# Kernel optimization log

Hardware: AMD Instinct MI355X
Metric: run time of the kernel (lower is better)

Reference implementation:

```python
import jax, jax.numpy as jnp
import numpy as np

E = 20000      # num edges
S = 64         # mul of 0e (scalar) channels
V = 32         # mul of 1o (vector) channels
FC_IN = 128    # radial basis length
HID = 64       # fc hidden width
INV_SQRT3 = 0.5773502691896258  # CG(1o x 1o -> 0e) = delta_ij / sqrt(3)


def setup_inputs() -> dict:
    key = jax.random.key(0)
    ks = jax.random.split(key, 16)
    n = jax.random.normal
    return {
        # edge features, layout [64 scalars | 32 vectors * 3 comps]
        "fea_in1": n(ks[0], (E, S + 3 * V), jnp.float32),
        "fea_in2": n(ks[1], (E, S + 3 * V), jnp.float32),
        "fea_weight": n(ks[2], (E, FC_IN), jnp.float32),
        # FullyConnectedTensorProduct internal weights (e3nn init: normal(0,1))
        "w_ss_s": n(ks[3], (S, S, S), jnp.float32),   # 0e x 0e -> 64x0e scalars
        "w_vv_s": n(ks[4], (V, V, S), jnp.float32),   # 1o x 1o -> 64x0e scalars
        "w_ss_g": n(ks[5], (S, S, V), jnp.float32),   # 0e x 0e -> 32x0e gates
        "w_vv_g": n(ks[6], (V, V, V), jnp.float32),   # 1o x 1o -> 32x0e gates
        "w_sv_v": n(ks[7], (S, V, V), jnp.float32),   # 0e x 1o -> 32x1o
        "w_vs_v": n(ks[8], (V, S, V), jnp.float32),   # 1o x 0e -> 32x1o
        # fc MLP: Linear(128,64) SiLU Linear(64,64) SiLU Linear(64,96)
        "fc_w1": n(ks[9], (FC_IN, HID), jnp.float32) / np.sqrt(FC_IN).astype(np.float32),
        "fc_b1": jnp.zeros((HID,), jnp.float32),
        "fc_w2": n(ks[10], (HID, HID), jnp.float32) / np.sqrt(HID).astype(np.float32),
        "fc_b2": jnp.zeros((HID,), jnp.float32),
        "fc_w3": n(ks[11], (HID, S + V), jnp.float32) / np.sqrt(HID).astype(np.float32),
        "fc_b3": jnp.zeros((S + V,), jnp.float32),
        "batch_edge": jnp.zeros((E,), jnp.int32),  # unused (norm='')
    }


def _equiconv(fea_in1, fea_in2, fea_weight,
              w_ss_s, w_vv_s, w_ss_g, w_vv_g, w_sv_v, w_vs_v,
              fc_w1, fc_b1, fc_w2, fc_b2, fc_w3, fc_b3):
    x1s, x1v = fea_in1[:, :S], fea_in1[:, S:].reshape(-1, V, 3)
    x2s, x2v = fea_in2[:, :S], fea_in2[:, S:].reshape(-1, V, 3)

    # path normalization: 1/sqrt(fan_in), fan_in = sum(mul1*mul2) over paths to output
    a_sc = 1.0 / np.sqrt(S * S + V * V).astype(np.float32)
    a_vec = 1.0 / np.sqrt(2 * S * V).astype(np.float32)

    # FullyConnectedTensorProduct (uvw connectivity)
    sc = a_sc * (jnp.einsum('eu,ev,uvw->ew', x1s, x2s, w_ss_s)
                 + INV_SQRT3 * jnp.einsum('eui,evi,uvw->ew', x1v, x2v, w_vv_s))
    g = a_sc * (jnp.einsum('eu,ev,uvw->ew', x1s, x2s, w_ss_g)
                + INV_SQRT3 * jnp.einsum('eui,evi,uvw->ew', x1v, x2v, w_vv_g))
    vec = a_vec * (jnp.einsum('eu,evi,uvw->ewi', x1s, x2v, w_sv_v)
                   + jnp.einsum('eui,ev,uvw->ewi', x1v, x2s, w_vs_v))

    # Gate: silu on scalars, sigmoid gates multiply the l>0 part
    sc = jax.nn.silu(sc)
    vec = vec * jax.nn.sigmoid(g)[:, :, None]

    # fc MLP producing per-channel elementwise conv weights
    h = jax.nn.silu(fea_weight @ fc_w1 + fc_b1)
    h = jax.nn.silu(h @ fc_w2 + fc_b2)
    w = h @ fc_w3 + fc_b3  # [E, S+V]

    # e3ElementWise: one scalar weight per channel (shared over m components)
    sc = sc * w[:, :S]
    vec = vec * w[:, S:, None]
    return jnp.concatenate([sc, vec.reshape(-1, 3 * V)], axis=-1)


def reference(fea_in1, fea_in2, fea_weight,
              w_ss_s, w_vv_s, w_ss_g, w_vv_g, w_sv_v, w_vs_v,
              fc_w1, fc_b1, fc_w2, fc_b2, fc_w3, fc_b3, batch_edge):
    del batch_edge  # only used by optional e3LayerNorm (norm='')
    return _equiconv(fea_in1, fea_in2, fea_weight,
                     w_ss_s, w_vv_s, w_ss_g, w_vv_g, w_sv_v, w_vs_v,
                     fc_w1, fc_b1, fc_w2, fc_b2, fc_w3, fc_b3)
```

## Files before the change

### kernel.cpp

```cpp
#include <hip/hip_runtime.h>


#define E_TOT 20000

typedef __attribute__((ext_vector_type(8))) short short8;
typedef __attribute__((ext_vector_type(4))) float f32x4;
typedef __attribute__((ext_vector_type(2))) __bf16 bf16x2;

#define FRAG_USH 512
#define CH_USH   3072
#define N_CH     52
#define STRIDE_W 159744
#define FC1_OFF  638976
#define FC2_OFF  647168
#define FC3_OFF  651264
#define WS_USH   657408

#define X1S_OFF  30720
#define X1V_OFF  34944
#define POOL_B   41216

__device__ __forceinline__ unsigned short f2b(float f){
  return __builtin_bit_cast(unsigned short, (__bf16)f);
}
__device__ __forceinline__ unsigned f2b2(float lo, float hi){
  bf16x2 t; t[0] = (__bf16)lo; t[1] = (__bf16)hi;
  return __builtin_bit_cast(unsigned, t);
}
__device__ __forceinline__ float b2f(unsigned short h){
  return __uint_as_float(((unsigned)h) << 16);
}
__device__ __forceinline__ float ulo(unsigned u){ return __uint_as_float(u << 16); }
__device__ __forceinline__ float uhi(unsigned u){ return __uint_as_float(u & 0xFFFF0000u); }
__device__ __forceinline__ f32x4 mfma16(short8 a, short8 b, f32x4 c){
  return __builtin_amdgcn_mfma_f32_16x16x32_bf16(a, b, c, 0, 0, 0);
}
union U8 { short8 v; unsigned u[4]; };
__device__ __forceinline__ float silu_f(float x){ return x/(1.f+__expf(-x)); }
__device__ __forceinline__ float sigm_f(float x){ return 1.f/(1.f+__expf(-x)); }

#define PACK8P(a, s, xp) { \
  a.u[0]=f2b2((s)*ulo((xp)[0]),(s)*uhi((xp)[0])); \
  a.u[1]=f2b2((s)*ulo((xp)[1]),(s)*uhi((xp)[1])); \
  a.u[2]=f2b2((s)*ulo((xp)[2]),(s)*uhi((xp)[2])); \
  a.u[3]=f2b2((s)*ulo((xp)[3]),(s)*uhi((xp)[3])); }

__device__ __forceinline__ int fpos(int kl, int n16){
  return (kl>>3)*128 + n16*8 + (kl&7);
}

__global__ void prep_weights(const float* __restrict__ ss_s, const float* __restrict__ ss_g,
                             const float* __restrict__ vv_s, const float* __restrict__ vv_g,
                             const float* __restrict__ sv,   const float* __restrict__ vs,
                             const float* __restrict__ w1,   const float* __restrict__ w2,
                             const float* __restrict__ w3,   unsigned short* __restrict__ wsb)
{
  int g = blockIdx.x * 256 + threadIdx.x;
  if (g >= WS_USH/8) return;
  const int dest = g << 3;
  const float A_SC  = 0.013975424859373686f;
  const float A_VV  = (float)(0.013975424859373686 * 0.5773502691896258);
  const float A_VEC = 0.015625f;

  const float* src = nullptr;
  int stride = 0;
  float scale = 1.f;

  if (dest < FC1_OFF) {
    int wave = dest / STRIDE_W;
    int off  = dest - wave*STRIDE_W;
    int c    = off / CH_USH;
    int rem  = off - c*CH_USH;
    int t    = rem >> 9;
    int p    = rem & 511;
    int kl   = (p >> 7) << 3;
    int n16  = (p >> 3) & 15;
    if (c < 32) {
      int u = (wave<<4) + (c>>1);
      int v = ((c&1)<<5) + kl;
      if (t < 4) { src = ss_s + (u<<12)+(v<<6)+((t<<4)+n16);     stride = 64; }
      else       { src = ss_g + (u<<11)+(v<<5)+(((t-4)<<4)+n16); stride = 32; }
      scale = A_SC;
    } else if (c < 40) {
      int u = (wave<<3) + (c-32);
      int v = kl;
      if (t < 4) { src = vv_s + (u<<11)+(v<<6)+((t<<4)+n16);     stride = 64; }
      else       { src = vv_g + (u<<10)+(v<<5)+(((t-4)<<4)+n16); stride = 32; }
      scale = A_VV;
    } else if (c < 46) {
      int ul = (c-40)*3 + (t>>1);
      if (ul < 16) {
        int u = (wave<<4) + ul;
        src = sv + (u<<10)+(kl<<5)+(((t&1)<<4)+n16);
        stride = 32; scale = A_VEC;
      }
    } else {
      int cc = c - 46;
      int vh = cc/3, ch3 = cc - vh*3;
      int fseq = ch3*6 + t;
      if (fseq < 16) {
        int u = (wave<<3) + (fseq>>1);
        int v = (vh<<5) + kl;
        src = vs + (u<<11)+(v<<5)+(((fseq&1)<<4)+n16);
        stride = 32; scale = A_VEC;
      }
    }
  } else if (dest < FC2_OFF) {
    int off = dest - FC1_OFF;
    int fi = off >> 9, p = off & 511;
    int kl = (p>>7)<<3, n16 = (p>>3)&15;
    int k = ((fi>>2)<<5) + kl, n = ((fi&3)<<4) + n16;
    src = w1 + (k<<6) + n; stride = 64;
  } else if (dest < FC3_OFF) {
    int off = dest - FC2_OFF;
    int fi = off >> 9, p = off & 511;
    int kl = (p>>7)<<3, n16 = (p>>3)&15;
    int k = ((fi>>2)<<5) + kl, n = ((fi&3)<<4) + n16;
    src = w2 + (k<<6) + n; stride = 64;
  } else {
    int off = dest - FC3_OFF;
    int fi = off >> 9, p = off & 511;
    int kl = (p>>7)<<3, n16 = (p>>3)&15;
    int koff = fi/6, nhi = fi - koff*6;
    int k = (koff<<5) + kl, n = (nhi<<4) + n16;
    src = w3 + k*96 + n; stride = 96;
  }

  U8 a;
  if (src) {
    float v0 = scale * src[0*stride], v1 = scale * src[1*stride];
    float v2 = scale * src[2*stride], v3 = scale * src[3*stride];
    float v4 = scale * src[4*stride], v5 = scale * src[5*stride];
    float v6 = scale * src[6*stride], v7 = scale * src[7*stride];
    a.u[0] = f2b2(v0, v1); a.u[1] = f2b2(v2, v3);
    a.u[2] = f2b2(v4, v5); a.u[3] = f2b2(v6, v7);
  } else {
    a.u[0] = 0; a.u[1] = 0; a.u[2] = 0; a.u[3] = 0;
  }
  *(short8*)(wsb + dest) = a.v;
}

__global__ __launch_bounds__(256, 2)
void equiconv_main(const float* __restrict__ fea1,
                   const float* __restrict__ fea2,
                   const float* __restrict__ few,
                   const float* __restrict__ fb1,
                   const float* __restrict__ fb2,
                   const float* __restrict__ fb3,
                   const unsigned short* __restrict__ wsb,
                   float* __restrict__ out)
{
  __shared__ __align__(16) unsigned char pool[POOL_B];
  float*          redf = (float*)pool;
  unsigned short* x1s_ = (unsigned short*)(pool + X1S_OFF);
  unsigned short* x1v_ = (unsigned short*)(pool + X1V_OFF);
  unsigned short* hb_  = (unsigned short*)(pool + X1S_OFF);

  #define X1S(r, cc) x1s_[(r)*66 + (cc)]
  #define X1V(r, cc) x1v_[(r)*98 + (cc)]
  #define HB(w, r, cc) hb_[(((w)<<4) + (r))*72 + (cc)]

  const int tid  = threadIdx.x;
  const int lane = tid & 63, wv = tid >> 6;
  const int ln   = lane & 15, quad = lane >> 4, q8 = quad << 3;
  const int ebase = blockIdx.x << 5;

  const int off16 = blockIdx.x & 15;
  const int off8  = blockIdx.x & 7;
  const int off6  = blockIdx.x % 6;

  for (int it = tid; it < 1280; it += 256){
    int row = it / 40, seg = it - row*40;
    float4 v1 = *(const float4*)(fea1 + (size_t)(ebase + row)*160 + seg*4);
    const float* p1 = (const float*)&v1;
    int c0 = seg*4;
    #pragma unroll
    for (int jj = 0; jj < 4; jj++){
      int col = c0 + jj;
      if (col < 64) X1S(row, col) = f2b(p1[jj]);
      else          X1V(row, col-64) = f2b(p1[jj]);
    }
  }
  __syncthreads();

  unsigned xep[2][4], xop[2][4], y0p[2][4], y1p[2][4], y2p[2][4];
  #pragma unroll
  for (int s = 0; s < 2; s++){
    const float* p = fea2 + (size_t)(ebase + s*16 + ln)*160;
    float4 a0 = *(const float4*)(p + q8);
    float4 a1 = *(const float4*)(p + q8 + 4);
    float4 b0 = *(const float4*)(p + 32 + q8);
    float4 b1 = *(const float4*)(p + 36 + q8);
    xep[s][0]=f2b2(a0.x,a0.y); xep[s][1]=f2b2(a0.z,a0.w);
    xep[s][2]=f2b2(a1.x,a1.y); xep[s][3]=f2b2(a1.z,a1.w);
    xop[s][0]=f2b2(b0.x,b0.y); xop[s][1]=f2b2(b0.z,b0.w);
    xop[s][2]=f2b2(b1.x,b1.y); xop[s][3]=f2b2(b1.z,b1.w);
    const float* py = p + 64 + q8*3;
    float yb[24];
    #pragma unroll
    for (int t = 0; t < 12; t++){
      float2 f2v = *(const float2*)(py + 2*t);
      yb[2*t] = f2v.x; yb[2*t+1] = f2v.y;
    }
    #pragma unroll
    for (int q = 0; q < 4; q++){
      y0p[s][q] = f2b2(yb[6*q+0], yb[6*q+3]);
      y1p[s][q] = f2b2(yb[6*q+1], yb[6*q+4]);
      y2p[s][q] = f2b2(yb[6*q+2], yb[6*q+5]);
    }
  }

  const unsigned short* gstream = wsb + (size_t)wv*STRIDE_W + lane*8;
  auto LD = [&](int c, short8* buf){
    const unsigned short* g = gstream + c*CH_USH;
    #pragma unroll
    for (int t = 0; t < 6; t++) buf[t] = *(const short8*)(g + t*FRAG_USH);
  };

  const int r0 = ln, r1 = 16 + ln;
  const f32x4 z4 = {0.f,0.f,0.f,0.f};
  f32x4 accS[2][6] = {{z4,z4,z4,z4,z4,z4},{z4,z4,z4,z4,z4,z4}};
  f32x4 accV[2][3][2] = {{{z4,z4},{z4,z4},{z4,z4}},{{z4,z4},{z4,z4},{z4,z4}}};

  short8 bA[6], bB[6];
  LD(2*off16, bA);

  #pragma unroll 1
  for (int i = 0; i < 16; i++){
    int p  = (i + off16) & 15;
    int pn = (i + 1 + off16) & 15;
    int u = (wv<<4) + p;
    float s0 = b2f(X1S(r0, u));
    float s1 = b2f(X1S(r1, u));
    {
      LD(2*p+1, bB);
      U8 a0, a1;
      PACK8P(a0, s0, xep[0]); PACK8P(a1, s1, xep[1]);
      #pragma unroll
      for (int t = 0; t < 6; t++){
        accS[0][t] = mfma16(a0.v, bA[t], accS[0][t]);
        accS[1][t] = mfma16(a1.v, bA[t], accS[1][t]);
      }
    }
    {
      int nextc = (i < 15) ? 2*pn : (32 + off8);
      LD(nextc, bA);
      U8 a0, a1;
      PACK8P(a0, s0, xop[0]); PACK8P(a1, s1, xop[1]);
      #pragma unroll
      for (int t = 0; t < 6; t++){
        accS[0][t] = mfma16(a0.v, bB[t], accS[0][t]);
        accS[1][t] = mfma16(a1.v, bB[t], accS[1][t]);
      }
    }
  }
  #define VVA(uV, s, aa) { \
    int rr = (s) ? r1 : r0; \
    float c0 = b2f(X1V(rr, (uV)*3+0)); \
    float c1 = b2f(X1V(rr, (uV)*3+1)); \
    float c2 = b2f(X1V(rr, (uV)*3+2)); \
    _Pragma("unroll") \
    for (int q = 0; q < 4; q++){ \
      float lo = c0*ulo(y0p[s][q]) + c1*ulo(y1p[s][q]) + c2*ulo(y2p[s][q]); \
      float hi = c0*uhi(y0p[s][q]) + c1*uhi(y1p[s][q]) + c2*uhi(y2p[s][q]); \
      aa.u[q] = f2b2(lo, hi); \
    } }
  #pragma unroll 1
  for (int j = 0; j < 8; j += 2){
    int k0 = (j + off8) & 7;
    int k1 = (j + 1 + off8) & 7;
    int k2 = (j + 2 + off8) & 7;
    {
      LD(32+k1, bB);
      int u = (wv<<3) + k0;
      U8 a0, a1; VVA(u, 0, a0); VVA(u, 1, a1);
      #pragma unroll
      for (int t = 0; t < 6; t++){
        accS[0][t] = mfma16(a0.v, bA[t], accS[0][t]);
        accS[1][t] = mfma16(a1.v, bA[t], accS[1][t]);
      }
    }
    {
      int nextc = (j < 6) ? (32 + k2) : (40 + off6);
      LD(nextc, bA);
      int u = (wv<<3) + k1;
      U8 a0, a1; VVA(u, 0, a0); VVA(u, 1, a1);
      #pragma unroll
      for (int t = 0; t < 6; t++){
        accS[0][t] = mfma16(a0.v, bB[t], accS[0][t]);
        accS[1][t] = mfma16(a1.v, bB[t], accS[1][t]);
      }
    }
  }
  #define SVBODY(chv, buf) { \
    _Pragma("unroll") \
    for (int uu = 0; uu < 3; uu++){ \
      int ui = (chv)*3 + uu; \
      if (ui < 16){ \
        int u = (wv<<4) + ui; \
        float s0 = b2f(X1S(r0, u)); \
        float s1 = b2f(X1S(r1, u)); \
        U8 a[2][3]; \
        PACK8P(a[0][0], s0, y0p[0]); PACK8P(a[0][1], s0, y1p[0]); PACK8P(a[0][2], s0, y2p[0]); \
        PACK8P(a[1][0], s1, y0p[1]); PACK8P(a[1][1], s1, y1p[1]); PACK8P(a[1][2], s1, y2p[1]); \
        _Pragma("unroll") \
        for (int t = 0; t < 2; t++){ \
          short8 b8 = buf[uu*2 + t]; \
          _Pragma("unroll") \
          for (int s = 0; s < 2; s++) \
            _Pragma("unroll") \
            for (int i2 = 0; i2 < 3; i2++) \
              accV[s][i2][t] = mfma16(a[s][i2].v, b8, accV[s][i2][t]); \
        } \
      } \
    } }
  #pragma unroll 1
  for (int j = 0; j < 6; j += 2){
    int c0i = j + off6;     if (c0i >= 6) c0i -= 6;
    int c1i = j + 1 + off6; if (c1i >= 6) c1i -= 6;
    int c2i = j + 2 + off6; if (c2i >= 6) c2i -= 6;
    { LD(40 + c1i, bB); SVBODY(c0i, bA); }
    {
      int nextc = (j < 4) ? (40 + c2i) : (46 + off6);
      LD(nextc, bA);
      SVBODY(c1i, bB);
    }
  }
  #define VSBODY(pcv, buf) { \
    const int p_ = (pcv)/3, ch_ = (pcv) - p_*3; \
    _Pragma("unroll") \
    for (int uu = 0; uu < 3; uu++){ \
      int ui = ch_*3 + uu; \
      if (ui < 8){ \
        int u = (wv<<3) + ui; \
        U8 a[2][3]; \
        _Pragma("unroll") \
        for (int s = 0; s < 2; s++){ \
          int rr = s ? r1 : r0; \
          float c0 = b2f(X1V(rr, u*3+0)); \
          float c1 = b2f(X1V(rr, u*3+1)); \
          float c2 = b2f(X1V(rr, u*3+2)); \
          const unsigned* xx = p_ ? xop[s] : xep[s]; \
          PACK8P(a[s][0], c0, xx); PACK8P(a[s][1], c1, xx); PACK8P(a[s][2], c2, xx); \
        } \
        _Pragma("unroll") \
        for (int t = 0; t < 2; t++){ \
          short8 b8 = buf[uu*2 + t]; \
          _Pragma("unroll") \
          for (int s = 0; s < 2; s++) \
            _Pragma("unroll") \
            for (int i2 = 0; i2 < 3; i2++) \
              accV[s][i2][t] = mfma16(a[s][i2].v, b8, accV[s][i2][t]); \
        } \
      } \
    } }
  #pragma unroll 1
  for (int j = 0; j < 6; j += 2){
    int c0i = j + off6;     if (c0i >= 6) c0i -= 6;
    int c1i = j + 1 + off6; if (c1i >= 6) c1i -= 6;
    int c2i = j + 2 + off6; if (c2i >= 6) c2i -= 6;
    { LD(46 + c1i, bB); VSBODY(c0i, bA); }
    {
      if (j < 4) LD(46 + c2i, bA);
      VSBODY(c1i, bB);
    }
  }

  f32x4 T0[12], T1[12];
  #pragma unroll
  for (int t = 0; t < 6; t++){ T0[t] = accS[0][t]; T1[t] = accS[1][t]; }
  #pragma unroll
  for (int t = 0; t < 2; t++)
    #pragma unroll
    for (int i = 0; i < 3; i++){
      T0[6+3*t+i] = accV[0][i][t]; T1[6+3*t+i] = accV[1][i][t];
    }

  #define PUT12(base, T) { _Pragma("unroll") for (int j=0;j<12;j++) \
    *(f32x4*)(redf + ((base)+j)*320 + ln*20 + (quad<<2)) = T[j]; }
  #define ADD12(base, T) { _Pragma("unroll") for (int j=0;j<12;j++) \
    T[j] += *(const f32x4*)(redf + ((base)+j)*320 + ln*20 + (quad<<2)); }

  __syncthreads();
  if (wv==1) PUT12(0, T0);  if (wv==2) PUT12(12, T1);
  __syncthreads();
  if (wv==0) ADD12(0, T0);  if (wv==3) ADD12(12, T1);
  __syncthreads();
  if (wv==2) PUT12(0, T0);  if (wv==1) PUT12(12, T1);
  __syncthreads();
  if (wv==0) ADD12(0, T0);  if (wv==3) ADD12(12, T1);
  __syncthreads();
  if (wv==3) PUT12(0, T0);  if (wv==0) PUT12(12, T1);
  __syncthreads();
  if (wv==0) ADD12(0, T0);  if (wv==3) ADD12(12, T1);

  if (wv == 1 || wv == 2) return;
  const int s = (wv == 0) ? 0 : 1;
  f32x4* P = (wv == 0) ? T0 : T1;

  f32x4 accF[4] = {z4,z4,z4,z4};
  {
    const float* fwp = few + (size_t)(ebase + s*16 + ln)*128;
    const short8* B = (const short8*)(wsb + FC1_OFF);
    #pragma unroll
    for (int c = 0; c < 4; c++){
      float4 fa  = *(const float4*)(fwp + c*32 + q8);
      float4 fbv = *(const float4*)(fwp + c*32 + q8 + 4);
      U8 a;
      a.u[0]=f2b2(fa.x,fa.y);   a.u[1]=f2b2(fa.z,fa.w);
      a.u[2]=f2b2(fbv.x,fbv.y); a.u[3]=f2b2(fbv.z,fbv.w);
      #pragma unroll
      for (int t = 0; t < 4; t++) accF[t] = mfma16(a.v, B[(c*4+t)*64 + lane], accF[t]);
    }
  }
  #pragma unroll
  for (int t = 0; t < 4; t++){
    float bb = fb1[(t<<4)+ln];
    #pragma unroll
    for (int r = 0; r < 4; r++)
      HB(wv, (quad<<2)+r, (t<<4)+ln) = f2b(silu_f(accF[t][r] + bb));
  }
  f32x4 acc2[4] = {z4,z4,z4,z4};
  {
    const short8* B = (const short8*)(wsb + FC2_OFF);
    #pragma unroll
    for (int c = 0; c < 2; c++){
      uint4 hq = *(const uint4*)&HB(wv, ln, c*32 + q8);
      U8 a; a.u[0]=hq.x; a.u[1]=hq.y; a.u[2]=hq.z; a.u[3]=hq.w;
      #pragma unroll
      for (int t = 0; t < 4; t++) acc2[t] = mfma16(a.v, B[(c*4+t)*64 + lane], acc2[t]);
    }
  }
  #pragma unroll
  for (int t = 0; t < 4; t++){
    float bb = fb2[(t<<4)+ln];
    #pragma unroll
    for (int r = 0; r < 4; r++)
      HB(wv, (quad<<2)+r, (t<<4)+ln) = f2b(silu_f(acc2[t][r] + bb));
  }
  f32x4 acc3[6] = {z4,z4,z4,z4,z4,z4};
  {
    const short8* B = (const short8*)(wsb + FC3_OFF);
    #pragma unroll
    for (int c = 0; c < 2; c++){
      uint4 hq = *(const uint4*)&HB(wv, ln, c*32 + q8);
      U8 a; a.u[0]=hq.x; a.u[1]=hq.y; a.u[2]=hq.z; a.u[3]=hq.w;
      #pragma unroll
      for (int t = 0; t < 6; t++) acc3[t] = mfma16(a.v, B[(c*6+t)*64 + lane], acc3[t]);
    }
  }

  #pragma unroll
  for (int r = 0; r < 4; r++){
    int eg = ebase + s*16 + (quad<<2) + r;
    float* op = out + (size_t)eg*160;
    #pragma unroll
    for (int t = 0; t < 4; t++)
      op[(t<<4)+ln] = silu_f(P[t][r]) * (acc3[t][r] + fb3[(t<<4)+ln]);
    #pragma unroll
    for (int tp = 0; tp < 2; tp++){
      int wc = (tp<<4) + ln;
      float f = sigm_f(P[4+tp][r]) * (acc3[4+tp][r] + fb3[64+wc]);
      op[64 + wc*3 + 0] = P[6+3*tp+0][r] * f;
      op[64 + wc*3 + 1] = P[6+3*tp+1][r] * f;
      op[64 + wc*3 + 2] = P[6+3*tp+2][r] * f;
    }
  }
}

extern "C" void kernel_launch(void* const* d_in, const int* in_sizes, int n_in,
                              void* d_out, int out_size, void* d_ws, size_t ws_size,
                              hipStream_t stream) {
  (void)in_sizes; (void)n_in; (void)out_size; (void)ws_size;
  unsigned short* wsb = (unsigned short*)d_ws;

  prep_weights<<<(WS_USH/8 + 255)/256, 256, 0, stream>>>(
      (const float*)d_in[3], (const float*)d_in[5],
      (const float*)d_in[4], (const float*)d_in[6],
      (const float*)d_in[7], (const float*)d_in[8],
      (const float*)d_in[9], (const float*)d_in[11], (const float*)d_in[13],
      wsb);

  equiconv_main<<<E_TOT/32, 256, 0, stream>>>(
      (const float*)d_in[0], (const float*)d_in[1], (const float*)d_in[2],
      (const float*)d_in[10], (const float*)d_in[12], (const float*)d_in[14],
      (const unsigned short*)wsb, (float*)d_out);
}
```

Measured before the change: 172.9 us.

## Reduce scalar accumulators early via LDS to cut registers, raise occupancy

The cross-wave reduction of the scalar-path accumulators now runs right after the scalar MFMA phase, before the vector phase. The reduced results are parked in spare LDS slots and reloaded at the end. This shortens the live range of the accumulators so register use can drop, and launch bounds go from 2 to 3 blocks per SIMD to raise occupancy. The cost is an extra round of barriers and LDS traffic, and spills are possible if the tighter register cap is too small.

```diff
diff --git a/kernel.cpp b/kernel.cpp
--- a/kernel.cpp
+++ b/kernel.cpp
@@ -140,7 +140,7 @@
   *(short8*)(wsb + dest) = a.v;
 }
 
-__global__ __launch_bounds__(256, 2)
+__global__ __launch_bounds__(256, 3)
 void equiconv_main(const float* __restrict__ fea1,
                    const float* __restrict__ fea2,
                    const float* __restrict__ few,
@@ -219,11 +219,11 @@
 
   const int r0 = ln, r1 = 16 + ln;
   const f32x4 z4 = {0.f,0.f,0.f,0.f};
-  f32x4 accS[2][6] = {{z4,z4,z4,z4,z4,z4},{z4,z4,z4,z4,z4,z4}};
-  f32x4 accV[2][3][2] = {{{z4,z4},{z4,z4},{z4,z4}},{{z4,z4},{z4,z4},{z4,z4}}};
 
   short8 bA[6], bB[6];
   LD(2*off16, bA);
+
+  f32x4 accS[2][6] = {{z4,z4,z4,z4,z4,z4},{z4,z4,z4,z4,z4,z4}};
 
   #pragma unroll 1
   for (int i = 0; i < 16; i++){
@@ -292,6 +292,29 @@
       }
     }
   }
+
+  #define PUT6(base, T) { _Pragma("unroll") for (int j=0;j<6;j++) \
+    *(f32x4*)(redf + ((base)+j)*320 + ln*20 + (quad<<2)) = T[j]; }
+  #define ADD6(base, T) { _Pragma("unroll") for (int j=0;j<6;j++) \
+    T[j] += *(const f32x4*)(redf + ((base)+j)*320 + ln*20 + (quad<<2)); }
+
+  __syncthreads();
+  if (wv==1) PUT6(0, accS[0]);  if (wv==2) PUT6(6, accS[1]);
+  __syncthreads();
+  if (wv==0) ADD6(0, accS[0]);  if (wv==3) ADD6(6, accS[1]);
+  __syncthreads();
+  if (wv==2) PUT6(0, accS[0]);  if (wv==1) PUT6(6, accS[1]);
+  __syncthreads();
+  if (wv==0) ADD6(0, accS[0]);  if (wv==3) ADD6(6, accS[1]);
+  __syncthreads();
+  if (wv==3) PUT6(0, accS[0]);  if (wv==0) PUT6(6, accS[1]);
+  __syncthreads();
+  if (wv==0) ADD6(0, accS[0]);  if (wv==3) ADD6(6, accS[1]);
+  if (wv==0) PUT6(12, accS[0]);
+  if (wv==3) { PUT6(18, accS[1]); }
+
+  f32x4 accV[2][3][2] = {{{z4,z4},{z4,z4},{z4,z4}},{{z4,z4},{z4,z4},{z4,z4}}};
+
   #define SVBODY(chv, buf) { \
     _Pragma("unroll") \
     for (int uu = 0; uu < 3; uu++){ \
@@ -366,37 +389,40 @@
     }
   }
 
-  f32x4 T0[12], T1[12];
-  #pragma unroll
-  for (int t = 0; t < 6; t++){ T0[t] = accS[0][t]; T1[t] = accS[1][t]; }
+  f32x4 V0[6], V1[6];
   #pragma unroll
   for (int t = 0; t < 2; t++)
     #pragma unroll
     for (int i = 0; i < 3; i++){
-      T0[6+3*t+i] = accV[0][i][t]; T1[6+3*t+i] = accV[1][i][t];
-    }
-
-  #define PUT12(base, T) { _Pragma("unroll") for (int j=0;j<12;j++) \
-    *(f32x4*)(redf + ((base)+j)*320 + ln*20 + (quad<<2)) = T[j]; }
-  #define ADD12(base, T) { _Pragma("unroll") for (int j=0;j<12;j++) \
-    T[j] += *(const f32x4*)(redf + ((base)+j)*320 + ln*20 + (quad<<2)); }
-
-  __syncthreads();
-  if (wv==1) PUT12(0, T0);  if (wv==2) PUT12(12, T1);
-  __syncthreads();
-  if (wv==0) ADD12(0, T0);  if (wv==3) ADD12(12, T1);
-  __syncthreads();
-  if (wv==2) PUT12(0, T0);  if (wv==1) PUT12(12, T1);
-  __syncthreads();
-  if (wv==0) ADD12(0, T0);  if (wv==3) ADD12(12, T1);
-  __syncthreads();
-  if (wv==3) PUT12(0, T0);  if (wv==0) PUT12(12, T1);
-  __syncthreads();
-  if (wv==0) ADD12(0, T0);  if (wv==3) ADD12(12, T1);
+      V0[3*t+i] = accV[0][i][t]; V1[3*t+i] = accV[1][i][t];
+    }
+
+  __syncthreads();
+  if (wv==1) PUT6(0, V0);  if (wv==2) PUT6(6, V1);
+  __syncthreads();
+  if (wv==0) ADD6(0, V0);  if (wv==3) ADD6(6, V1);
+  __syncthreads();
+  if (wv==2) PUT6(0, V0);  if (wv==1) PUT6(6, V1);
+  __syncthreads();
+  if (wv==0) ADD6(0, V0);  if (wv==3) ADD6(6, V1);
+  __syncthreads();
+  if (wv==3) PUT6(0, V0);  if (wv==0) PUT6(6, V1);
+  __syncthreads();
+  if (wv==0) ADD6(0, V0);  if (wv==3) ADD6(6, V1);
 
   if (wv == 1 || wv == 2) return;
   const int s = (wv == 0) ? 0 : 1;
-  f32x4* P = (wv == 0) ? T0 : T1;
+
+  f32x4 P[12];
+  {
+    const int sb = (wv == 0) ? 12 : 18;
+    #pragma unroll
+    for (int j = 0; j < 6; j++)
+      P[j] = *(const f32x4*)(redf + (sb+j)*320 + ln*20 + (quad<<2));
+    #pragma unroll
+    for (int j = 0; j < 6; j++)
+      P[6+j] = (wv == 0) ? V0[j] : V1[j];
+  }
 
   f32x4 accF[4] = {z4,z4,z4,z4};
   {
```

New measurement: 183.9 us. 6.4% more time.

## Process 64 edges per block to reuse streamed weight fragments across four subtiles

Applied to the files above, without the earlier changes.

Each block now handles 64 edges (four 16-row subtiles) instead of 32, so every weight fragment streamed from global memory feeds twice as many MFMAs. fea_in2 is staged into shared memory in bf16 (scalars and de-interleaved vector components) rather than held in registers. The cross-wave reduction is split into scalar and vector phases so that all four waves finish the MLP and epilogue for one subtile each. In exchange, shared memory grows to about 76 KB, accumulator register pressure doubles (which may hurt occupancy under launch_bounds 256,2), and the grid halves to 313 blocks with a clamped tail.

```diff
diff --git a/kernel.cpp b/kernel.cpp
--- a/kernel.cpp
+++ b/kernel.cpp
@@ -17,8 +17,10 @@
 #define WS_USH   657408
 
 #define X1S_OFF  30720
-#define X1V_OFF  34944
-#define POOL_B   41216
+#define X1V_OFF  39168
+#define X2S_OFF  51712
+#define Y_OFF    60928
+#define POOL_B   76288
 
 __device__ __forceinline__ unsigned short f2b(float f){
   return __builtin_bit_cast(unsigned short, (__bf16)f);
@@ -30,8 +32,6 @@
 __device__ __forceinline__ float b2f(unsigned short h){
   return __uint_as_float(((unsigned)h) << 16);
 }
-__device__ __forceinline__ float ulo(unsigned u){ return __uint_as_float(u << 16); }
-__device__ __forceinline__ float uhi(unsigned u){ return __uint_as_float(u & 0xFFFF0000u); }
 __device__ __forceinline__ f32x4 mfma16(short8 a, short8 b, f32x4 c){
   return __builtin_amdgcn_mfma_f32_16x16x32_bf16(a, b, c, 0, 0, 0);
 }
@@ -39,11 +39,11 @@
 __device__ __forceinline__ float silu_f(float x){ return x/(1.f+__expf(-x)); }
 __device__ __forceinline__ float sigm_f(float x){ return 1.f/(1.f+__expf(-x)); }
 
-#define PACK8P(a, s, xp) { \
-  a.u[0]=f2b2((s)*ulo((xp)[0]),(s)*uhi((xp)[0])); \
-  a.u[1]=f2b2((s)*ulo((xp)[1]),(s)*uhi((xp)[1])); \
-  a.u[2]=f2b2((s)*ulo((xp)[2]),(s)*uhi((xp)[2])); \
-  a.u[3]=f2b2((s)*ulo((xp)[3]),(s)*uhi((xp)[3])); }
+#define PACK8L(a, sc, f) { \
+  a.u[0]=f2b2((sc)*b2f((unsigned short)(f)[0]),(sc)*b2f((unsigned short)(f)[1])); \
+  a.u[1]=f2b2((sc)*b2f((unsigned short)(f)[2]),(sc)*b2f((unsigned short)(f)[3])); \
+  a.u[2]=f2b2((sc)*b2f((unsigned short)(f)[4]),(sc)*b2f((unsigned short)(f)[5])); \
+  a.u[3]=f2b2((sc)*b2f((unsigned short)(f)[6]),(sc)*b2f((unsigned short)(f)[7])); }
 
 __device__ __forceinline__ int fpos(int kl, int n16){
   return (kl>>3)*128 + n16*8 + (kl&7);
@@ -154,6 +154,8 @@
   float*          redf = (float*)pool;
   unsigned short* x1s_ = (unsigned short*)(pool + X1S_OFF);
   unsigned short* x1v_ = (unsigned short*)(pool + X1V_OFF);
+  unsigned short* x2s_ = (unsigned short*)(pool + X2S_OFF);
+  unsigned short* y_   = (unsigned short*)(pool + Y_OFF);
   unsigned short* hb_  = (unsigned short*)(pool + X1S_OFF);
 
   #define X1S(r, cc) x1s_[(r)*66 + (cc)]
@@ -163,52 +165,36 @@
   const int tid  = threadIdx.x;
   const int lane = tid & 63, wv = tid >> 6;
   const int ln   = lane & 15, quad = lane >> 4, q8 = quad << 3;
-  const int ebase = blockIdx.x << 5;
+  const int ebase = blockIdx.x << 6;
+  const int nsub  = min(4, (E_TOT - ebase) >> 4);
 
   const int off16 = blockIdx.x & 15;
   const int off8  = blockIdx.x & 7;
   const int off6  = blockIdx.x % 6;
 
-  for (int it = tid; it < 1280; it += 256){
+  for (int it = tid; it < 2560; it += 256){
     int row = it / 40, seg = it - row*40;
-    float4 v1 = *(const float4*)(fea1 + (size_t)(ebase + row)*160 + seg*4);
+    int er = ebase + row; if (er > E_TOT-1) er = E_TOT-1;
+    float4 v1 = *(const float4*)(fea1 + (size_t)er*160 + seg*4);
+    float4 v2 = *(const float4*)(fea2 + (size_t)er*160 + seg*4);
     const float* p1 = (const float*)&v1;
+    const float* p2 = (const float*)&v2;
     int c0 = seg*4;
     #pragma unroll
     for (int jj = 0; jj < 4; jj++){
       int col = c0 + jj;
-      if (col < 64) X1S(row, col) = f2b(p1[jj]);
-      else          X1V(row, col-64) = f2b(p1[jj]);
+      if (col < 64){
+        X1S(row, col) = f2b(p1[jj]);
+        x2s_[row*72 + col] = f2b(p2[jj]);
+      } else {
+        int vc = col - 64;
+        X1V(row, vc) = f2b(p1[jj]);
+        int vv = vc/3, ii = vc - vv*3;
+        y_[ii*2560 + row*40 + vv] = f2b(p2[jj]);
+      }
     }
   }
   __syncthreads();
-
-  unsigned xep[2][4], xop[2][4], y0p[2][4], y1p[2][4], y2p[2][4];
-  #pragma unroll
-  for (int s = 0; s < 2; s++){
-    const float* p = fea2 + (size_t)(ebase + s*16 + ln)*160;
-    float4 a0 = *(const float4*)(p + q8);
-    float4 a1 = *(const float4*)(p + q8 + 4);
-    float4 b0 = *(const float4*)(p + 32 + q8);
-    float4 b1 = *(const float4*)(p + 36 + q8);
-    xep[s][0]=f2b2(a0.x,a0.y); xep[s][1]=f2b2(a0.z,a0.w);
-    xep[s][2]=f2b2(a1.x,a1.y); xep[s][3]=f2b2(a1.z,a1.w);
-    xop[s][0]=f2b2(b0.x,b0.y); xop[s][1]=f2b2(b0.z,b0.w);
-    xop[s][2]=f2b2(b1.x,b1.y); xop[s][3]=f2b2(b1.z,b1.w);
-    const float* py = p + 64 + q8*3;
-    float yb[24];
-    #pragma unroll
-    for (int t = 0; t < 12; t++){
-      float2 f2v = *(const float2*)(py + 2*t);
-      yb[2*t] = f2v.x; yb[2*t+1] = f2v.y;
-    }
-    #pragma unroll
-    for (int q = 0; q < 4; q++){
-      y0p[s][q] = f2b2(yb[6*q+0], yb[6*q+3]);
-      y1p[s][q] = f2b2(yb[6*q+1], yb[6*q+4]);
-      y2p[s][q] = f2b2(yb[6*q+2], yb[6*q+5]);
-    }
-  }
 
   const unsigned short* gstream = wsb + (size_t)wv*STRIDE_W + lane*8;
   auto LD = [&](int c, short8* buf){
@@ -217,100 +203,147 @@
     for (int t = 0; t < 6; t++) buf[t] = *(const short8*)(g + t*FRAG_USH);
   };
 
-  const int r0 = ln, r1 = 16 + ln;
   const f32x4 z4 = {0.f,0.f,0.f,0.f};
-  f32x4 accS[2][6] = {{z4,z4,z4,z4,z4,z4},{z4,z4,z4,z4,z4,z4}};
-  f32x4 accV[2][3][2] = {{{z4,z4},{z4,z4},{z4,z4}},{{z4,z4},{z4,z4},{z4,z4}}};
-
   short8 bA[6], bB[6];
   LD(2*off16, bA);
+
+  f32x4 accS[4][6];
+  #pragma unroll
+  for (int s = 0; s < 4; s++)
+    #pragma unroll
+    for (int t = 0; t < 6; t++) accS[s][t] = z4;
 
   #pragma unroll 1
   for (int i = 0; i < 16; i++){
     int p  = (i + off16) & 15;
     int pn = (i + 1 + off16) & 15;
     int u = (wv<<4) + p;
-    float s0 = b2f(X1S(r0, u));
-    float s1 = b2f(X1S(r1, u));
+    float sc[4];
+    #pragma unroll
+    for (int s = 0; s < 4; s++) sc[s] = b2f(X1S(s*16+ln, u));
     {
       LD(2*p+1, bB);
-      U8 a0, a1;
-      PACK8P(a0, s0, xep[0]); PACK8P(a1, s1, xep[1]);
       #pragma unroll
-      for (int t = 0; t < 6; t++){
-        accS[0][t] = mfma16(a0.v, bA[t], accS[0][t]);
-        accS[1][t] = mfma16(a1.v, bA[t], accS[1][t]);
+      for (int s = 0; s < 4; s++){
+        short8 xf = *(const short8*)&x2s_[(s*16+ln)*72 + q8];
+        U8 a; PACK8L(a, sc[s], xf);
+        #pragma unroll
+        for (int t = 0; t < 6; t++) accS[s][t] = mfma16(a.v, bA[t], accS[s][t]);
       }
     }
     {
       int nextc = (i < 15) ? 2*pn : (32 + off8);
       LD(nextc, bA);
-      U8 a0, a1;
-      PACK8P(a0, s0, xop[0]); PACK8P(a1, s1, xop[1]);
       #pragma unroll
-      for (int t = 0; t < 6; t++){
-        accS[0][t] = mfma16(a0.v, bB[t], accS[0][t]);
-        accS[1][t] = mfma16(a1.v, bB[t], accS[1][t]);
+      for (int s = 0; s < 4; s++){
+        short8 xf = *(const short8*)&x2s_[(s*16+ln)*72 + 32 + q8];
+        U8 a; PACK8L(a, sc[s], xf);
+        #pragma unroll
+        for (int t = 0; t < 6; t++) accS[s][t] = mfma16(a.v, bB[t], accS[s][t]);
       }
     }
   }
-  #define VVA(uV, s, aa) { \
-    int rr = (s) ? r1 : r0; \
-    float c0 = b2f(X1V(rr, (uV)*3+0)); \
-    float c1 = b2f(X1V(rr, (uV)*3+1)); \
-    float c2 = b2f(X1V(rr, (uV)*3+2)); \
+
+  short8 y0f[4], y1f[4], y2f[4];
+  #pragma unroll
+  for (int s = 0; s < 4; s++){
+    y0f[s] = *(const short8*)&y_[0*2560 + (s*16+ln)*40 + q8];
+    y1f[s] = *(const short8*)&y_[1*2560 + (s*16+ln)*40 + q8];
+    y2f[s] = *(const short8*)&y_[2*2560 + (s*16+ln)*40 + q8];
+  }
+
+  #define VVBODY(kk, buf) { \
+    int u_ = (wv<<3) + (kk); \
     _Pragma("unroll") \
-    for (int q = 0; q < 4; q++){ \
-      float lo = c0*ulo(y0p[s][q]) + c1*ulo(y1p[s][q]) + c2*ulo(y2p[s][q]); \
-      float hi = c0*uhi(y0p[s][q]) + c1*uhi(y1p[s][q]) + c2*uhi(y2p[s][q]); \
-      aa.u[q] = f2b2(lo, hi); \
+    for (int s = 0; s < 4; s++){ \
+      float c0 = b2f(X1V(s*16+ln, u_*3+0)); \
+      float c1 = b2f(X1V(s*16+ln, u_*3+1)); \
+      float c2 = b2f(X1V(s*16+ln, u_*3+2)); \
+      U8 a; \
+      _Pragma("unroll") \
+      for (int q = 0; q < 4; q++){ \
+        float lo = c0*b2f((unsigned short)y0f[s][2*q])   + c1*b2f((unsigned short)y1f[s][2*q])   + c2*b2f((unsigned short)y2f[s][2*q]); \
+        float hi = c0*b2f((unsigned short)y0f[s][2*q+1]) + c1*b2f((unsigned short)y1f[s][2*q+1]) + c2*b2f((unsigned short)y2f[s][2*q+1]); \
+        a.u[q] = f2b2(lo, hi); \
+      } \
+      _Pragma("unroll") \
+      for (int t = 0; t < 6; t++) accS[s][t] = mfma16(a.v, buf[t], accS[s][t]); \
     } }
   #pragma unroll 1
   for (int j = 0; j < 8; j += 2){
     int k0 = (j + off8) & 7;
     int k1 = (j + 1 + off8) & 7;
     int k2 = (j + 2 + off8) & 7;
-    {
-      LD(32+k1, bB);
-      int u = (wv<<3) + k0;
-      U8 a0, a1; VVA(u, 0, a0); VVA(u, 1, a1);
-      #pragma unroll
-      for (int t = 0; t < 6; t++){
-        accS[0][t] = mfma16(a0.v, bA[t], accS[0][t]);
-        accS[1][t] = mfma16(a1.v, bA[t], accS[1][t]);
-      }
-    }
+    { LD(32+k1, bB); VVBODY(k0, bA); }
     {
       int nextc = (j < 6) ? (32 + k2) : (40 + off6);
       LD(nextc, bA);
-      int u = (wv<<3) + k1;
-      U8 a0, a1; VVA(u, 0, a0); VVA(u, 1, a1);
-      #pragma unroll
-      for (int t = 0; t < 6; t++){
-        accS[0][t] = mfma16(a0.v, bB[t], accS[0][t]);
-        accS[1][t] = mfma16(a1.v, bB[t], accS[1][t]);
-      }
-    }
-  }
+      VVBODY(k1, bB);
+    }
+  }
+
+  #define PUTS(ACC, sub) { _Pragma("unroll") for (int j=0;j<6;j++) \
+    *(f32x4*)(redf + ((sub)*6+j)*320 + ln*20 + (quad<<2)) = ACC[sub][j]; }
+  #define ADDS(ACC, o)   { _Pragma("unroll") for (int j=0;j<6;j++) \
+    ACC[o][j] += *(const f32x4*)(redf + ((o)*6+j)*320 + ln*20 + (quad<<2)); }
+  #define REDUCE4(ACC) { \
+    if (wv==0) PUTS(ACC,3) if (wv==1) PUTS(ACC,0) if (wv==2) PUTS(ACC,1) if (wv==3) PUTS(ACC,2) \
+    __syncthreads(); \
+    if (wv==0) ADDS(ACC,0) if (wv==1) ADDS(ACC,1) if (wv==2) ADDS(ACC,2) if (wv==3) ADDS(ACC,3) \
+    __syncthreads(); \
+    if (wv==0) PUTS(ACC,2) if (wv==1) PUTS(ACC,3) if (wv==2) PUTS(ACC,0) if (wv==3) PUTS(ACC,1) \
+    __syncthreads(); \
+    if (wv==0) ADDS(ACC,0) if (wv==1) ADDS(ACC,1) if (wv==2) ADDS(ACC,2) if (wv==3) ADDS(ACC,3) \
+    __syncthreads(); \
+    if (wv==0) PUTS(ACC,1) if (wv==1) PUTS(ACC,2) if (wv==2) PUTS(ACC,3) if (wv==3) PUTS(ACC,0) \
+    __syncthreads(); \
+    if (wv==0) ADDS(ACC,0) if (wv==1) ADDS(ACC,1) if (wv==2) ADDS(ACC,2) if (wv==3) ADDS(ACC,3) }
+
+  __syncthreads();
+  REDUCE4(accS);
+  f32x4 Sfin[6];
+  if (wv==0){
+    #pragma unroll
+    for (int j=0;j<6;j++) Sfin[j]=accS[0][j];
+  }
+  if (wv==1){
+    #pragma unroll
+    for (int j=0;j<6;j++) Sfin[j]=accS[1][j];
+  }
+  if (wv==2){
+    #pragma unroll
+    for (int j=0;j<6;j++) Sfin[j]=accS[2][j];
+  }
+  if (wv==3){
+    #pragma unroll
+    for (int j=0;j<6;j++) Sfin[j]=accS[3][j];
+  }
+  __syncthreads();
+
+  f32x4 accV[4][6];
+  #pragma unroll
+  for (int s = 0; s < 4; s++)
+    #pragma unroll
+    for (int t = 0; t < 6; t++) accV[s][t] = z4;
+
   #define SVBODY(chv, buf) { \
     _Pragma("unroll") \
     for (int uu = 0; uu < 3; uu++){ \
       int ui = (chv)*3 + uu; \
       if (ui < 16){ \
-        int u = (wv<<4) + ui; \
-        float s0 = b2f(X1S(r0, u)); \
-        float s1 = b2f(X1S(r1, u)); \
-        U8 a[2][3]; \
-        PACK8P(a[0][0], s0, y0p[0]); PACK8P(a[0][1], s0, y1p[0]); PACK8P(a[0][2], s0, y2p[0]); \
-        PACK8P(a[1][0], s1, y0p[1]); PACK8P(a[1][1], s1, y1p[1]); PACK8P(a[1][2], s1, y2p[1]); \
+        int u_ = (wv<<4) + ui; \
         _Pragma("unroll") \
-        for (int t = 0; t < 2; t++){ \
-          short8 b8 = buf[uu*2 + t]; \
+        for (int s = 0; s < 4; s++){ \
+          float scs = b2f(X1S(s*16+ln, u_)); \
+          U8 a0, a1, a2; \
+          PACK8L(a0, scs, y0f[s]); PACK8L(a1, scs, y1f[s]); PACK8L(a2, scs, y2f[s]); \
           _Pragma("unroll") \
-          for (int s = 0; s < 2; s++) \
-            _Pragma("unroll") \
-            for (int i2 = 0; i2 < 3; i2++) \
-              accV[s][i2][t] = mfma16(a[s][i2].v, b8, accV[s][i2][t]); \
+          for (int t = 0; t < 2; t++){ \
+            short8 b8 = buf[uu*2 + t]; \
+            accV[s][t*3+0] = mfma16(a0.v, b8, accV[s][t*3+0]); \
+            accV[s][t*3+1] = mfma16(a1.v, b8, accV[s][t*3+1]); \
+            accV[s][t*3+2] = mfma16(a2.v, b8, accV[s][t*3+2]); \
+          } \
         } \
       } \
     } }
@@ -332,25 +365,22 @@
     for (int uu = 0; uu < 3; uu++){ \
       int ui = ch_*3 + uu; \
       if (ui < 8){ \
-        int u = (wv<<3) + ui; \
-        U8 a[2][3]; \
+        int u_ = (wv<<3) + ui; \
         _Pragma("unroll") \
-        for (int s = 0; s < 2; s++){ \
-          int rr = s ? r1 : r0; \
-          float c0 = b2f(X1V(rr, u*3+0)); \
-          float c1 = b2f(X1V(rr, u*3+1)); \
-          float c2 = b2f(X1V(rr, u*3+2)); \
-          const unsigned* xx = p_ ? xop[s] : xep[s]; \
-          PACK8P(a[s][0], c0, xx); PACK8P(a[s][1], c1, xx); PACK8P(a[s][2], c2, xx); \
-        } \
-        _Pragma("unroll") \
-        for (int t = 0; t < 2; t++){ \
-          short8 b8 = buf[uu*2 + t]; \
+        for (int s = 0; s < 4; s++){ \
+          float c0 = b2f(X1V(s*16+ln, u_*3+0)); \
+          float c1 = b2f(X1V(s*16+ln, u_*3+1)); \
+          float c2 = b2f(X1V(s*16+ln, u_*3+2)); \
+          short8 xf = *(const short8*)&x2s_[(s*16+ln)*72 + p_*32 + q8]; \
+          U8 a0, a1, a2; \
+          PACK8L(a0, c0, xf); PACK8L(a1, c1, xf); PACK8L(a2, c2, xf); \
           _Pragma("unroll") \
-          for (int s = 0; s < 2; s++) \
-            _Pragma("unroll") \
-            for (int i2 = 0; i2 < 3; i2++) \
-              accV[s][i2][t] = mfma16(a[s][i2].v, b8, accV[s][i2][t]); \
+          for (int t = 0; t < 2; t++){ \
+            short8 b8 = buf[uu*2 + t]; \
+            accV[s][t*3+0] = mfma16(a0.v, b8, accV[s][t*3+0]); \
+            accV[s][t*3+1] = mfma16(a1.v, b8, accV[s][t*3+1]); \
+            accV[s][t*3+2] = mfma16(a2.v, b8, accV[s][t*3+2]); \
+          } \
         } \
       } \
     } }
@@ -366,41 +396,34 @@
     }
   }
 
-  f32x4 T0[12], T1[12];
-  #pragma unroll
-  for (int t = 0; t < 6; t++){ T0[t] = accS[0][t]; T1[t] = accS[1][t]; }
-  #pragma unroll
-  for (int t = 0; t < 2; t++)
-    #pragma unroll
-    for (int i = 0; i < 3; i++){
-      T0[6+3*t+i] = accV[0][i][t]; T1[6+3*t+i] = accV[1][i][t];
-    }
-
-  #define PUT12(base, T) { _Pragma("unroll") for (int j=0;j<12;j++) \
-    *(f32x4*)(redf + ((base)+j)*320 + ln*20 + (quad<<2)) = T[j]; }
-  #define ADD12(base, T) { _Pragma("unroll") for (int j=0;j<12;j++) \
-    T[j] += *(const f32x4*)(redf + ((base)+j)*320 + ln*20 + (quad<<2)); }
-
-  __syncthreads();
-  if (wv==1) PUT12(0, T0);  if (wv==2) PUT12(12, T1);
-  __syncthreads();
-  if (wv==0) ADD12(0, T0);  if (wv==3) ADD12(12, T1);
-  __syncthreads();
-  if (wv==2) PUT12(0, T0);  if (wv==1) PUT12(12, T1);
-  __syncthreads();
-  if (wv==0) ADD12(0, T0);  if (wv==3) ADD12(12, T1);
-  __syncthreads();
-  if (wv==3) PUT12(0, T0);  if (wv==0) PUT12(12, T1);
-  __syncthreads();
-  if (wv==0) ADD12(0, T0);  if (wv==3) ADD12(12, T1);
-
-  if (wv == 1 || wv == 2) return;
-  const int s = (wv == 0) ? 0 : 1;
-  f32x4* P = (wv == 0) ? T0 : T1;
+  REDUCE4(accV);
+  f32x4 Vfin[6];
+  if (wv==0){
+    #pragma unroll
+    for (int j=0;j<6;j++) Vfin[j]=accV[0][j];
+  }
+  if (wv==1){
+    #pragma unroll
+    for (int j=0;j<6;j++) Vfin[j]=accV[1][j];
+  }
+  if (wv==2){
+    #pragma unroll
+    for (int j=0;j<6;j++) Vfin[j]=accV[2][j];
+  }
+  if (wv==3){
+    #pragma unroll
+    for (int j=0;j<6;j++) Vfin[j]=accV[3][j];
+  }
+
+  if (wv >= nsub) return;
+
+  f32x4 P[12];
+  #pragma unroll
+  for (int j = 0; j < 6; j++){ P[j] = Sfin[j]; P[6+j] = Vfin[j]; }
 
   f32x4 accF[4] = {z4,z4,z4,z4};
   {
-    const float* fwp = few + (size_t)(ebase + s*16 + ln)*128;
+    const float* fwp = few + (size_t)(ebase + wv*16 + ln)*128;
     const short8* B = (const short8*)(wsb + FC1_OFF);
     #pragma unroll
     for (int c = 0; c < 4; c++){
@@ -452,7 +475,7 @@
 
   #pragma unroll
   for (int r = 0; r < 4; r++){
-    int eg = ebase + s*16 + (quad<<2) + r;
+    int eg = ebase + wv*16 + (quad<<2) + r;
     float* op = out + (size_t)eg*160;
     #pragma unroll
     for (int t = 0; t < 4; t++)
@@ -481,7 +504,7 @@
       (const float*)d_in[9], (const float*)d_in[11], (const float*)d_in[13],
       wsb);
 
-  equiconv_main<<<E_TOT/32, 256, 0, stream>>>(
+  equiconv_main<<<(E_TOT + 63)/64, 256, 0, stream>>>(
       (const float*)d_in[0], (const float*)d_in[1], (const float*)d_in[2],
       (const float*)d_in[10], (const float*)d_in[12], (const float*)d_in[14],
       (const unsigned short*)wsb, (float*)d_out);
```

Result: slower. 228.1 us (+32.0%).
